# Kernel tuning notes

Hardware: AMD Instinct MI355X
Metric: run time of the kernel (lower is better)

## Reference

```python
import jax, jax.numpy as jnp
import numpy as np

NS, NC, T, NB = 32, 16, 64, 512
NSC = NS + NC


def setup_inputs() -> dict:
    key = jax.random.key(0)
    k1, k2, k3, k4, k5 = jax.random.split(key, 5)
    # SPD cost matrices so Quu is invertible (as assumed by the LQR math)
    L = jax.random.normal(k1, (NB, T, NSC, NSC), jnp.float32) * 0.1
    Q = L @ jnp.swapaxes(L, -1, -2) + jnp.eye(NSC, dtype=jnp.float32)
    p = jax.random.normal(k2, (NB, T, NSC), jnp.float32)
    x_init = jax.random.normal(k3, (NB, NS), jnp.float32)
    # stable-ish LTI dynamics
    A = 0.9 * jnp.eye(NS, dtype=jnp.float32) + 0.01 * jax.random.normal(k4, (NS, NS), jnp.float32)
    B = 0.1 * jax.random.normal(k5, (NS, NC), jnp.float32)
    dt = jnp.float32(0.1)
    return {"x_init": x_init, "Q": Q, "p": p, "A": A, "B": B, "dt": dt}


def _lqr(x_init, Q, p, A, B):
    ns, nc = A.shape[0], B.shape[1]
    nb, Th = Q.shape[0], Q.shape[1]
    dtype = Q.dtype

    # --- nominal rollout with zero control: x_{t+1} = A x_t ---
    def roll(x, _):
        return x @ A.T, x
    _, cx = jax.lax.scan(roll, x_init, None, length=Th)   # [T,B,ns] states x_0..x_{T-1}
    cu = jnp.zeros((Th, nb, nc), dtype)                    # current_u = 0
    xu = jnp.concatenate([cx, cu], -1)                     # [T,B,nsc]

    Qs = jnp.swapaxes(Q, 0, 1)                             # [T,B,nsc,nsc]
    ps = jnp.swapaxes(p, 0, 1)                             # [T,B,nsc]
    p_new = jnp.einsum('tbij,tbj->tbi', Qs, xu) + ps       # [T,B,nsc]

    F = jnp.concatenate([A, B], axis=1)                    # [ns, nsc]

    # --- backward Riccati recursion (V=v=0 at t=T-1 makes Qt=Q[T-1]) ---
    def bwd(carry, inp):
        V, v = carry                                       # [B,ns,ns], [B,ns]
        Qt_in, qt_in = inp
        Qt = Qt_in + jnp.einsum('si,bst,tj->bij', F, V, F)
        qt = qt_in + v @ F                                 # F^T v
        Qxx, Qxu = Qt[:, :ns, :ns], Qt[:, :ns, ns:]
        Qux, Quu = Qt[:, ns:, :ns], Qt[:, ns:, ns:]
        qx, qu = qt[:, :ns], qt[:, ns:]
        Quu_inv = jnp.linalg.pinv(Quu)
        Kt = -Quu_inv @ Qux                                # [B,nc,ns]
        kt = -jnp.einsum('bij,bj->bi', Quu_inv, qu)        # [B,nc]
        KtT = jnp.swapaxes(Kt, -1, -2)
        Vn = Qxx + Qxu @ Kt + KtT @ Qux + KtT @ Quu @ Kt
        vn = (qx + jnp.einsum('bij,bj->bi', Qxu, kt)
              + jnp.einsum('bij,bj->bi', KtT, qu)
              + jnp.einsum('bij,bj->bi', KtT @ Quu, kt))
        return (Vn, vn), (Kt, kt)

    V0 = jnp.zeros((nb, ns, ns), dtype)
    v0 = jnp.zeros((nb, ns), dtype)
    _, (Ks, ks) = jax.lax.scan(bwd, (V0, v0), (Qs, p_new), reverse=True)

    # --- forward rollout with feedback policy ---
    def fwd(carry, inp):
        xt, cost = carry
        Kt, kt, cxt, cut, Qt, pt = inp
        dut = jnp.einsum('bij,bj->bi', Kt, xt - cxt) + kt
        ut = dut + cut
        xut = jnp.concatenate([xt, ut], -1)
        cost = cost + 0.5 * jnp.einsum('bi,bij,bj->b', xut, Qt, xut) + (xut * pt).sum(-1)
        xn = xt @ A.T + ut @ B.T
        return (xn, cost), (xt, ut)

    (_, cost), (xs, us) = jax.lax.scan(
        fwd, (x_init, jnp.zeros(nb, dtype)), (Ks, ks, cx, cu, Qs, ps))
    x = jnp.swapaxes(xs, 0, 1)   # [B,T,ns]  (states x_0..x_{T-1}, matching x[...,:-1,:])
    u = jnp.swapaxes(us, 0, 1)   # [B,T,nc]
    return x, u, cost


def reference(x_init, Q, p, A, B, dt):
    # dt only matters for nonlinear relinearization; with constant LTI (A,B) it is unused.
    return _lqr(x_init, Q, p, A, B)
```

## Files before the change

### kernel.cpp

```cpp
#include <hip/hip_runtime.h>


#define NSd 32
#define NCd 16
#define Td 64
#define NBd 512
#define SQS 52
#define TP 40
#define FP 20

typedef __bf16 bf16x8 __attribute__((ext_vector_type(8)));
typedef __bf16 bf16x4 __attribute__((ext_vector_type(4)));
typedef float f32x4 __attribute__((ext_vector_type(4)));

#define MFMA16(a, b, c) __builtin_amdgcn_mfma_f32_16x16x32_bf16(a, b, c, 0, 0, 0)

#define XOFF ((size_t)0)
#define UOFF ((size_t)NBd * Td * NSd)
#define COFF (UOFF + (size_t)NBd * Td * NCd)

__device__ __forceinline__ float rdl(float v, int l) {
  return __uint_as_float(__builtin_amdgcn_readlane(__float_as_uint(v), l));
}

__device__ __forceinline__ void bar_lgkm() {
  asm volatile("s_waitcnt lgkmcnt(0)\n\ts_barrier" ::: "memory");
}

struct BW {
  __bf16 FTh[48][TP], FTl[48][TP];
  __bf16 WTh[48][TP], WTl[48][TP];
  __bf16 Xh[32][TP], Xl[32][TP];
  __bf16 KTh[32][TP], KTl[32][TP];
  __bf16 XTh[16][TP], XTl[16][TP];
  __bf16 S2h[48][TP], S2l[48][TP];
  float S1T[6][16][FP];
  float QdT[3][16][FP];
  float Qd1R[16][FP];
  float QuuT[16][FP];
  float qt[48];
  float vv[32];
};
struct FW {
  float K2T[2][16 * 36];
  float kv2[2][16];
  float d[32];
  float xs[32];
  float uu[16];
};
union LdsU {
  BW bw;
  FW fw;
};

#define SQSTORE(i, v)                            \
  do {                                           \
    int _r = (i) / 12, _c = (i) - _r * 12;       \
    *(float4*)&sQ[_r * SQS + _c * 4] = (v);      \
  } while (0)

__global__ __launch_bounds__(256, 2) void lqr_kernel(
    const float* __restrict__ x_init, const float* __restrict__ Qg,
    const float* __restrict__ pg, const float* __restrict__ Ag,
    const float* __restrict__ Bg, float* __restrict__ out,
    float* __restrict__ wsK, float* __restrict__ wskv) {
  const int b = blockIdx.x;
  const int tid = threadIdx.x;
  const int w = tid >> 6;
  const int lane = tid & 63;
  const int fn = lane & 15;
  const int quad = lane >> 4;
  const int k0 = quad * 8;

  __shared__ __attribute__((aligned(16))) float sQ[48 * SQS];
  __shared__ __attribute__((aligned(16))) float scx[Td][NSd];
  __shared__ __attribute__((aligned(16))) float sFf[NSd][SQS];
  __shared__ __attribute__((aligned(16))) LdsU U;
  __shared__ float scostp[1];

  for (int idx = tid; idx < 1536; idx += 256) {
    int i = idx / 48, j = idx - i * 48;
    sFf[i][j] = (j < 32) ? Ag[i * 32 + j] : Bg[i * 16 + (j - 32)];
  }
  for (int idx = tid; idx < 1536; idx += 256) {
    int a = idx >> 5, k = idx & 31;
    float f = (a < 32) ? Ag[k * 32 + a] : Bg[k * 16 + (a - 32)];
    __bf16 h = (__bf16)f;
    U.bw.FTh[a][k] = h;
    U.bw.FTl[a][k] = (__bf16)(f - (float)h);
  }
  for (int idx = tid; idx < 1536; idx += 256) {
    int r = idx >> 5, c = idx & 31;
    __bf16 z = (__bf16)0.f;
    U.bw.S2h[r][c] = z;
    U.bw.S2l[r][c] = z;
    if (r < 32) {
      U.bw.KTh[r][c] = z;
      U.bw.KTl[r][c] = z;
    }
  }
  for (int idx = tid; idx < 6 * 16 * FP; idx += 256) ((float*)U.bw.S1T)[idx] = 0.f;
  if (tid < 32) {
    scx[0][tid] = x_init[b * 32 + tid];
    U.bw.vv[tid] = 0.f;
  }
  {
    const float4* src = (const float4*)(Qg + ((size_t)b * Td + 63) * 2304);
    float4 v0 = src[tid];
    float4 v1 = src[tid + 256];
    SQSTORE(tid, v0);
    SQSTORE(tid + 256, v1);
    if (tid < 64) {
      float4 v2 = src[tid + 512];
      SQSTORE(tid + 512, v2);
    }
  }
  float ppf = 0.f;
  if (w == 3 && lane < 48) ppf = pg[((size_t)b * Td + 63) * 48 + lane];
  __syncthreads();

  if (w == 0) {
    for (int t2 = 0; t2 < Td - 1; ++t2) {
      if (lane < 32) {
        float acc = 0.f;
#pragma unroll
        for (int j = 0; j < 32; j += 4) {
          float4 a4 = *(const float4*)&sFf[lane][j];
          acc += a4.x * scx[t2][j] + a4.y * scx[t2][j + 1] +
                 a4.z * scx[t2][j + 2] + a4.w * scx[t2][j + 3];
        }
        scx[t2 + 1][lane] = acc;
      }
    }
  }
  __syncthreads();

  float cAcc = 0.f;
  float dAcc = 0.f;

  for (int t = Td - 1; t >= 0; --t) {
    float4 pf0, pf1, pf2;
    float ppfn;
    if (t > 0) {
      if (w < 3) {
        const float4* src = (const float4*)(Qg + ((size_t)b * Td + (t - 1)) * 2304);
        pf0 = src[tid];
        pf1 = src[tid + 192];
        pf2 = src[tid + 384];
      } else if (lane < 48) {
        ppfn = pg[((size_t)b * Td + t - 1) * 48 + lane];
      }
    }

    if (w < 3) {
      const int I = w;
      {
        bf16x8 aH = *(const bf16x8*)&U.bw.S2h[16 * I + fn][k0];
        bf16x8 aL = *(const bf16x8*)&U.bw.S2l[16 * I + fn][k0];
#pragma unroll
        for (int J = 0; J < 2; ++J) {
          bf16x8 bH = *(const bf16x8*)&U.bw.KTh[16 * J + fn][k0];
          bf16x8 bL = *(const bf16x8*)&U.bw.KTl[16 * J + fn][k0];
          float4 s1 = *(const float4*)&U.bw.S1T[I * 2 + J][fn][4 * quad];
          f32x4 acc = {s1.x, s1.y, s1.z, s1.w};
          acc = MFMA16(aL, bH, acc);
          acc = MFMA16(aH, bL, acc);
          acc = MFMA16(aH, bH, acc);
#pragma unroll
          for (int r = 0; r < 4; ++r) {
            float v = acc[r];
            __bf16 h = (__bf16)v;
            U.bw.WTh[16 * I + 4 * quad + r][16 * J + fn] = h;
            U.bw.WTl[16 * I + 4 * quad + r][16 * J + fn] = (__bf16)(v - (float)h);
          }
        }
      }
      bf16x8 wH = *(const bf16x8*)&U.bw.WTh[16 * I + fn][k0];
      bf16x8 wL = *(const bf16x8*)&U.bw.WTl[16 * I + fn][k0];
      if (I == 2) {
        bf16x8 bH = *(const bf16x8*)&U.bw.FTh[32 + fn][k0];
        bf16x8 bL = *(const bf16x8*)&U.bw.FTl[32 + fn][k0];
        f32x4 acc;
#pragma unroll
        for (int r = 0; r < 4; ++r)
          acc[r] = sQ[(32 + 4 * quad + r) * SQS + 32 + fn];
        acc = MFMA16(wL, bH, acc);
        acc = MFMA16(wH, bL, acc);
        acc = MFMA16(wH, bH, acc);
        float4 st = {acc[0], acc[1], acc[2], acc[3]};
        *(float4*)&U.bw.QuuT[fn][4 * quad] = st;
      } else {
        {
          bf16x8 bH = *(const bf16x8*)&U.bw.FTh[16 * I + fn][k0];
          bf16x8 bL = *(const bf16x8*)&U.bw.FTl[16 * I + fn][k0];
          f32x4 acc;
#pragma unroll
          for (int r = 0; r < 4; ++r)
            acc[r] = sQ[(16 * I + 4 * quad + r) * SQS + 16 * I + fn];
          acc = MFMA16(wL, bH, acc);
          acc = MFMA16(wH, bL, acc);
          acc = MFMA16(wH, bH, acc);
          float4 st = {acc[0], acc[1], acc[2], acc[3]};
          *(float4*)&U.bw.QdT[I * 2][fn][4 * quad] = st;
        }
        if (I == 0) {
          bf16x8 bH = *(const bf16x8*)&U.bw.FTh[16 + fn][k0];
          bf16x8 bL = *(const bf16x8*)&U.bw.FTl[16 + fn][k0];
          f32x4 acc;
#pragma unroll
          for (int r = 0; r < 4; ++r)
            acc[r] = sQ[(4 * quad + r) * SQS + 16 + fn];
          acc = MFMA16(wL, bH, acc);
          acc = MFMA16(wH, bL, acc);
          acc = MFMA16(wH, bH, acc);
          float4 st = {acc[0], acc[1], acc[2], acc[3]};
          *(float4*)&U.bw.QdT[1][fn][4 * quad] = st;
#pragma unroll
          for (int r = 0; r < 4; ++r) U.bw.Qd1R[4 * quad + r][fn] = acc[r];
        }
        {
          bf16x8 bH = *(const bf16x8*)&U.bw.FTh[32 + fn][k0];
          bf16x8 bL = *(const bf16x8*)&U.bw.FTl[32 + fn][k0];
          f32x4 acc;
#pragma unroll
          for (int r = 0; r < 4; ++r)
            acc[r] = sQ[(16 * I + 4 * quad + r) * SQS + 32 + fn];
          acc = MFMA16(wL, bH, acc);
          acc = MFMA16(wH, bL, acc);
          acc = MFMA16(wH, bH, acc);
          bf16x4 th, tl;
#pragma unroll
          for (int r = 0; r < 4; ++r) {
            float v = acc[r];
            __bf16 h = (__bf16)v;
            __bf16 l = (__bf16)(v - (float)h);
            U.bw.Xh[16 * I + 4 * quad + r][fn] = h;
            U.bw.Xl[16 * I + 4 * quad + r][fn] = l;
            th[r] = h;
            tl[r] = l;
          }
          *(bf16x4*)&U.bw.XTh[fn][16 * I + 4 * quad] = th;
          *(bf16x4*)&U.bw.XTl[fn][16 * I + 4 * quad] = tl;
        }
      }
    } else if (lane < 48) {
      float acc1 = ppf;
#pragma unroll
      for (int k = 0; k < 32; ++k) acc1 += sQ[k * SQS + lane] * scx[t][k];
      if (lane < 32) cAcc += 0.5f * scx[t][lane] * (acc1 + ppf);
      float acc = acc1;
#pragma unroll
      for (int k = 0; k < 32; ++k) acc += U.bw.vv[k] * sFf[k][lane];
      U.bw.qt[lane] = acc;
    }
    bar_lgkm();

    if (t > 0) {
      if (w < 3) {
        SQSTORE(tid, pf0);
        SQSTORE(tid + 192, pf1);
        SQSTORE(tid + 384, pf2);
      } else if (lane < 48) {
        ppf = ppfn;
      }
    }
    if (w < 3 && t > 0) {
      const int I = w;
      bf16x8 aH = *(const bf16x8*)&U.bw.FTh[16 * I + fn][k0];
      bf16x8 aL = *(const bf16x8*)&U.bw.FTl[16 * I + fn][k0];
#pragma unroll
      for (int J = 0; J < 2; ++J) {
        const float* bsrc;
        if (J == 0)
          bsrc = (quad < 2) ? &U.bw.QdT[0][fn][0] : &U.bw.Qd1R[fn][0];
        else
          bsrc = (quad < 2) ? &U.bw.QdT[1][fn][0] : &U.bw.QdT[2][fn][0];
        const int off = (quad & 1) * 8;
        float4 c0 = *(const float4*)&bsrc[off];
        float4 c1 = *(const float4*)&bsrc[off + 4];
        float bf[8] = {c0.x, c0.y, c0.z, c0.w, c1.x, c1.y, c1.z, c1.w};
        bf16x8 bH, bL;
#pragma unroll
        for (int j = 0; j < 8; ++j) {
          __bf16 h = (__bf16)bf[j];
          bH[j] = h;
          bL[j] = (__bf16)(bf[j] - (float)h);
        }
        f32x4 acc = {0.f, 0.f, 0.f, 0.f};
        acc = MFMA16(aL, bH, acc);
        acc = MFMA16(aH, bL, acc);
        acc = MFMA16(aH, bH, acc);
        float4 st = {acc[0], acc[1], acc[2], acc[3]};
        *(float4*)&U.bw.S1T[I * 2 + J][fn][4 * quad] = st;
      }
      {
        bf16x8 bH = *(const bf16x8*)&U.bw.XTh[fn][k0];
        bf16x8 bL = *(const bf16x8*)&U.bw.XTl[fn][k0];
        f32x4 acc = {0.f, 0.f, 0.f, 0.f};
        acc = MFMA16(aL, bH, acc);
        acc = MFMA16(aH, bL, acc);
        acc = MFMA16(aH, bH, acc);
#pragma unroll
        for (int r = 0; r < 4; ++r) {
          float v = acc[r];
          __bf16 h = (__bf16)v;
          U.bw.S2h[16 * I + 4 * quad + r][fn] = h;
          U.bw.S2l[16 * I + 4 * quad + r][fn] = (__bf16)(v - (float)h);
        }
      }
    }
    if (w == 3) {
      float rhs[16];
      if (lane < 32) {
        bf16x8 xh0 = *(const bf16x8*)&U.bw.Xh[lane][0];
        bf16x8 xh1 = *(const bf16x8*)&U.bw.Xh[lane][8];
        bf16x8 xl0 = *(const bf16x8*)&U.bw.Xl[lane][0];
        bf16x8 xl1 = *(const bf16x8*)&U.bw.Xl[lane][8];
#pragma unroll
        for (int i = 0; i < 8; ++i) {
          rhs[i] = (float)xh0[i] + (float)xl0[i];
          rhs[8 + i] = (float)xh1[i] + (float)xl1[i];
        }
      } else {
#pragma unroll
        for (int i = 0; i < 16; ++i) rhs[i] = U.bw.qt[32 + i];
      }
      float quu[16];
      *(float4*)&quu[0] = *(const float4*)&U.bw.QuuT[fn][0];
      *(float4*)&quu[4] = *(const float4*)&U.bw.QuuT[fn][4];
      *(float4*)&quu[8] = *(const float4*)&U.bw.QuuT[fn][8];
      *(float4*)&quu[12] = *(const float4*)&U.bw.QuuT[fn][12];
      float inv[16];
#pragma unroll
      for (int r = 0; r < 15; ++r) {
        inv[r] = __builtin_amdgcn_rcpf(rdl(quu[r], r));
#pragma unroll
        for (int i = r + 1; i < 16; ++i) {
          float m = rdl(quu[i], r) * inv[r];
          rhs[i] -= m * rhs[r];
          quu[i] -= m * quu[r];
        }
      }
      inv[15] = __builtin_amdgcn_rcpf(rdl(quu[15], 15));
      float xx[16];
#pragma unroll
      for (int r = 15; r >= 0; --r) {
        float s = rhs[r];
#pragma unroll
        for (int c = r + 1; c < 16; ++c) s -= rdl(quu[r], c) * xx[c];
        xx[r] = s * inv[r];
      }
      if (lane < 32) {
        bf16x8 h0, l0, h1, l1;
#pragma unroll
        for (int u = 0; u < 8; ++u) {
          float kv = -xx[u];
          __bf16 hh = (__bf16)kv;
          h0[u] = hh;
          l0[u] = (__bf16)(kv - (float)hh);
          float kv2 = -xx[8 + u];
          __bf16 hh2 = (__bf16)kv2;
          h1[u] = hh2;
          l1[u] = (__bf16)(kv2 - (float)hh2);
        }
        *(bf16x8*)&U.bw.KTh[lane][0] = h0;
        *(bf16x8*)&U.bw.KTh[lane][8] = h1;
        *(bf16x8*)&U.bw.KTl[lane][0] = l0;
        *(bf16x8*)&U.bw.KTl[lane][8] = l1;
        float4* dst = (float4*)(wsK + (((size_t)b * Td + t) * 32 + lane) * 16);
        float4 v0 = {-xx[0], -xx[1], -xx[2], -xx[3]};
        float4 v1 = {-xx[4], -xx[5], -xx[6], -xx[7]};
        float4 v2 = {-xx[8], -xx[9], -xx[10], -xx[11]};
        float4 v3 = {-xx[12], -xx[13], -xx[14], -xx[15]};
        dst[0] = v0; dst[1] = v1; dst[2] = v2; dst[3] = v3;
      } else if (lane == 32) {
        float4* dst = (float4*)(wskv + ((size_t)b * Td + t) * 16);
        float4 v0 = {-xx[0], -xx[1], -xx[2], -xx[3]};
        float4 v1 = {-xx[4], -xx[5], -xx[6], -xx[7]};
        float4 v2 = {-xx[8], -xx[9], -xx[10], -xx[11]};
        float4 v3 = {-xx[12], -xx[13], -xx[14], -xx[15]};
        dst[0] = v0; dst[1] = v1; dst[2] = v2; dst[3] = v3;
        float s = 0.f;
#pragma unroll
        for (int i = 0; i < 16; ++i) s += U.bw.qt[32 + i] * xx[i];
        dAcc -= 0.5f * s;
      }
      {
        float acc = 0.f;
        bf16x8 xh0, xh1, xl0, xl1;
        if (lane < 32) {
          xh0 = *(const bf16x8*)&U.bw.Xh[lane][0];
          xh1 = *(const bf16x8*)&U.bw.Xh[lane][8];
          xl0 = *(const bf16x8*)&U.bw.Xl[lane][0];
          xl1 = *(const bf16x8*)&U.bw.Xl[lane][8];
          acc = U.bw.qt[lane];
        }
#pragma unroll
        for (int u = 0; u < 8; ++u) {
          float kt0 = -rdl(xx[u], 32);
          float kt1 = -rdl(xx[8 + u], 32);
          if (lane < 32) {
            acc += ((float)xh0[u] + (float)xl0[u]) * kt0;
            acc += ((float)xh1[u] + (float)xl1[u]) * kt1;
          }
        }
        if (lane < 32) U.bw.vv[lane] = acc;
      }
    }
    bar_lgkm();
  }

  if (w == 3) {
    float rv = (lane < 32) ? cAcc : (lane == 32 ? dAcc : 0.f);
    rv += __shfl_down(rv, 32);
    rv += __shfl_down(rv, 16);
    rv += __shfl_down(rv, 8);
    rv += __shfl_down(rv, 4);
    rv += __shfl_down(rv, 2);
    rv += __shfl_down(rv, 1);
    if (lane == 0) scostp[0] = rv;
  }
  __syncthreads();

  if (w == 0) {
    {
      const float4* src = (const float4*)(wsK + ((size_t)b * Td) * 512);
      float4 ka = src[lane * 2], kb = src[lane * 2 + 1];
      int jj = lane >> 1, ib = (lane & 1) * 8;
      float* kt2 = U.fw.K2T[0];
      kt2[(ib + 0) * 36 + jj] = ka.x; kt2[(ib + 1) * 36 + jj] = ka.y;
      kt2[(ib + 2) * 36 + jj] = ka.z; kt2[(ib + 3) * 36 + jj] = ka.w;
      kt2[(ib + 4) * 36 + jj] = kb.x; kt2[(ib + 5) * 36 + jj] = kb.y;
      kt2[(ib + 6) * 36 + jj] = kb.z; kt2[(ib + 7) * 36 + jj] = kb.w;
      if (lane < 16) U.fw.kv2[0][lane] = wskv[(size_t)b * Td * 16 + lane];
    }
    float xr = (lane < 32) ? scx[0][lane] : 0.f;
    for (int t = 0; t < Td; ++t) {
      const int cur = t & 1, nxt = cur ^ 1;
      float4 pa, pb;
      float pk;
      if (t < Td - 1) {
        const float4* src = (const float4*)(wsK + ((size_t)b * Td + t + 1) * 512);
        pa = src[lane * 2];
        pb = src[lane * 2 + 1];
        if (lane < 16) pk = wskv[((size_t)b * Td + t + 1) * 16 + lane];
      }
      if (lane < 32) {
        U.fw.d[lane] = xr - scx[t][lane];
        U.fw.xs[lane] = xr;
        out[XOFF + ((size_t)b * Td + t) * 32 + lane] = xr;
      }
      if (lane < 16) {
        float uv = U.fw.kv2[cur][lane];
        const float* kr = &U.fw.K2T[cur][lane * 36];
#pragma unroll
        for (int j4 = 0; j4 < 8; ++j4) {
          float4 kk = *(const float4*)&kr[j4 * 4];
          float4 dd = *(const float4*)&U.fw.d[j4 * 4];
          uv += kk.x * dd.x + kk.y * dd.y + kk.z * dd.z + kk.w * dd.w;
        }
        U.fw.uu[lane] = uv;
        out[UOFF + ((size_t)b * Td + t) * 16 + lane] = uv;
      }
      if (lane < 32) {
        float acc = 0.f;
#pragma unroll
        for (int j4 = 0; j4 < 8; ++j4) {
          float4 ff = *(const float4*)&sFf[lane][j4 * 4];
          float4 xv = *(const float4*)&U.fw.xs[j4 * 4];
          acc += ff.x * xv.x + ff.y * xv.y + ff.z * xv.z + ff.w * xv.w;
        }
#pragma unroll
        for (int j4 = 0; j4 < 4; ++j4) {
          float4 ff = *(const float4*)&sFf[lane][32 + j4 * 4];
          float4 uv = *(const float4*)&U.fw.uu[j4 * 4];
          acc += ff.x * uv.x + ff.y * uv.y + ff.z * uv.z + ff.w * uv.w;
        }
        xr = acc;
      }
      if (t < Td - 1) {
        int jj = lane >> 1, ib = (lane & 1) * 8;
        float* kt2 = U.fw.K2T[nxt];
        kt2[(ib + 0) * 36 + jj] = pa.x; kt2[(ib + 1) * 36 + jj] = pa.y;
        kt2[(ib + 2) * 36 + jj] = pa.z; kt2[(ib + 3) * 36 + jj] = pa.w;
        kt2[(ib + 4) * 36 + jj] = pb.x; kt2[(ib + 5) * 36 + jj] = pb.y;
        kt2[(ib + 6) * 36 + jj] = pb.z; kt2[(ib + 7) * 36 + jj] = pb.w;
        if (lane < 16) U.fw.kv2[nxt][lane] = pk;
      }
    }
    if (lane == 0) out[COFF + b] = scostp[0];
  }
}

extern "C" void kernel_launch(void* const* d_in, const int* in_sizes, int n_in,
                              void* d_out, int out_size, void* d_ws, size_t ws_size,
                              hipStream_t stream) {
  const float* x_init = (const float*)d_in[0];
  const float* Qg = (const float*)d_in[1];
  const float* pg = (const float*)d_in[2];
  const float* Ag = (const float*)d_in[3];
  const float* Bg = (const float*)d_in[4];
  float* out = (float*)d_out;
  float* wsK = (float*)d_ws;
  float* wskv = wsK + (size_t)NBd * Td * NSd * NCd;
  lqr_kernel<<<NBd, 256, 0, stream>>>(x_init, Qg, pg, Ag, Bg, out, wsK, wskv);
}
```

Before: 620.8 us.

## Rotate wave roles per block and hoist loop-invariant MFMA operands into registers

Wave roles are rotated by a block-dependent shift so the serial solver wave lands on different SIMDs across co-resident blocks. Loop-invariant bf16 F^T fragments, F columns, and the carried S1/S2 fragments are kept in registers instead of being reloaded from LDS each step. The solver wave also gets raised priority, the q-vector is read once into registers, and the sQ access is vectorized. The v update is rewritten algebraically from Qxu*k to a dot of the solve result with qu. This adds register pressure, and the v-update algebra depends on what xx holds for lanes below 32.

```diff
diff --git a/kernel.cpp b/kernel.cpp
--- a/kernel.cpp
+++ b/kernel.cpp
@@ -71,6 +71,8 @@
   const int fn = lane & 15;
   const int quad = lane >> 4;
   const int k0 = quad * 8;
+  const int shift = (b ^ (b >> 8)) & 3;
+  const int rw = (w + shift) & 3;
 
   __shared__ __attribute__((aligned(16))) float sQ[48 * SQS];
   __shared__ __attribute__((aligned(16))) float scx[Td][NSd];
@@ -116,10 +118,10 @@
     }
   }
   float ppf = 0.f;
-  if (w == 3 && lane < 48) ppf = pg[((size_t)b * Td + 63) * 48 + lane];
+  if (rw == 3 && lane < 48) ppf = pg[((size_t)b * Td + 63) * 48 + lane];
   __syncthreads();
 
-  if (w == 0) {
+  if (rw == 0) {
     for (int t2 = 0; t2 < Td - 1; ++t2) {
       if (lane < 32) {
         float acc = 0.f;
@@ -135,6 +137,23 @@
   }
   __syncthreads();
 
+  const int I3 = (rw < 3) ? rw : 0;
+  bf16x8 hFTdH = *(const bf16x8*)&U.bw.FTh[16 * I3 + fn][k0];
+  bf16x8 hFTdL = *(const bf16x8*)&U.bw.FTl[16 * I3 + fn][k0];
+  bf16x8 hFT1H = *(const bf16x8*)&U.bw.FTh[16 + fn][k0];
+  bf16x8 hFT1L = *(const bf16x8*)&U.bw.FTl[16 + fn][k0];
+  bf16x8 hFT2H = *(const bf16x8*)&U.bw.FTh[32 + fn][k0];
+  bf16x8 hFT2L = *(const bf16x8*)&U.bw.FTl[32 + fn][k0];
+  bf16x8 hS2H = *(const bf16x8*)&U.bw.S2h[16 * I3 + fn][k0];
+  bf16x8 hS2L = *(const bf16x8*)&U.bw.S2l[16 * I3 + fn][k0];
+  float4 hS1a = *(const float4*)&U.bw.S1T[I3 * 2 + 0][fn][4 * quad];
+  float4 hS1b = *(const float4*)&U.bw.S1T[I3 * 2 + 1][fn][4 * quad];
+  float fcol[32];
+  if (rw == 3 && lane < 48) {
+#pragma unroll
+    for (int k = 0; k < 32; ++k) fcol[k] = sFf[k][lane];
+  }
+
   float cAcc = 0.f;
   float dAcc = 0.f;
 
@@ -142,30 +161,29 @@
     float4 pf0, pf1, pf2;
     float ppfn;
     if (t > 0) {
-      if (w < 3) {
+      if (rw < 3) {
+        const int ptid = rw * 64 + lane;
         const float4* src = (const float4*)(Qg + ((size_t)b * Td + (t - 1)) * 2304);
-        pf0 = src[tid];
-        pf1 = src[tid + 192];
-        pf2 = src[tid + 384];
+        pf0 = src[ptid];
+        pf1 = src[ptid + 192];
+        pf2 = src[ptid + 384];
       } else if (lane < 48) {
         ppfn = pg[((size_t)b * Td + t - 1) * 48 + lane];
       }
     }
 
-    if (w < 3) {
-      const int I = w;
+    if (rw < 3) {
+      const int I = rw;
       {
-        bf16x8 aH = *(const bf16x8*)&U.bw.S2h[16 * I + fn][k0];
-        bf16x8 aL = *(const bf16x8*)&U.bw.S2l[16 * I + fn][k0];
 #pragma unroll
         for (int J = 0; J < 2; ++J) {
           bf16x8 bH = *(const bf16x8*)&U.bw.KTh[16 * J + fn][k0];
           bf16x8 bL = *(const bf16x8*)&U.bw.KTl[16 * J + fn][k0];
-          float4 s1 = *(const float4*)&U.bw.S1T[I * 2 + J][fn][4 * quad];
+          float4 s1 = (J == 0) ? hS1a : hS1b;
           f32x4 acc = {s1.x, s1.y, s1.z, s1.w};
-          acc = MFMA16(aL, bH, acc);
-          acc = MFMA16(aH, bL, acc);
-          acc = MFMA16(aH, bH, acc);
+          acc = MFMA16(hS2L, bH, acc);
+          acc = MFMA16(hS2H, bL, acc);
+          acc = MFMA16(hS2H, bH, acc);
 #pragma unroll
           for (int r = 0; r < 4; ++r) {
             float v = acc[r];
@@ -178,56 +196,50 @@
       bf16x8 wH = *(const bf16x8*)&U.bw.WTh[16 * I + fn][k0];
       bf16x8 wL = *(const bf16x8*)&U.bw.WTl[16 * I + fn][k0];
       if (I == 2) {
-        bf16x8 bH = *(const bf16x8*)&U.bw.FTh[32 + fn][k0];
-        bf16x8 bL = *(const bf16x8*)&U.bw.FTl[32 + fn][k0];
         f32x4 acc;
 #pragma unroll
         for (int r = 0; r < 4; ++r)
           acc[r] = sQ[(32 + 4 * quad + r) * SQS + 32 + fn];
-        acc = MFMA16(wL, bH, acc);
-        acc = MFMA16(wH, bL, acc);
-        acc = MFMA16(wH, bH, acc);
+        acc = MFMA16(wL, hFT2H, acc);
+        acc = MFMA16(wH, hFT2L, acc);
+        acc = MFMA16(wH, hFT2H, acc);
         float4 st = {acc[0], acc[1], acc[2], acc[3]};
         *(float4*)&U.bw.QuuT[fn][4 * quad] = st;
       } else {
         {
-          bf16x8 bH = *(const bf16x8*)&U.bw.FTh[16 * I + fn][k0];
-          bf16x8 bL = *(const bf16x8*)&U.bw.FTl[16 * I + fn][k0];
+          bf16x8 dH = (I == 0) ? hFTdH : hFT1H;
+          bf16x8 dL = (I == 0) ? hFTdL : hFT1L;
           f32x4 acc;
 #pragma unroll
           for (int r = 0; r < 4; ++r)
             acc[r] = sQ[(16 * I + 4 * quad + r) * SQS + 16 * I + fn];
-          acc = MFMA16(wL, bH, acc);
-          acc = MFMA16(wH, bL, acc);
-          acc = MFMA16(wH, bH, acc);
+          acc = MFMA16(wL, dH, acc);
+          acc = MFMA16(wH, dL, acc);
+          acc = MFMA16(wH, dH, acc);
           float4 st = {acc[0], acc[1], acc[2], acc[3]};
           *(float4*)&U.bw.QdT[I * 2][fn][4 * quad] = st;
         }
         if (I == 0) {
-          bf16x8 bH = *(const bf16x8*)&U.bw.FTh[16 + fn][k0];
-          bf16x8 bL = *(const bf16x8*)&U.bw.FTl[16 + fn][k0];
           f32x4 acc;
 #pragma unroll
           for (int r = 0; r < 4; ++r)
             acc[r] = sQ[(4 * quad + r) * SQS + 16 + fn];
-          acc = MFMA16(wL, bH, acc);
-          acc = MFMA16(wH, bL, acc);
-          acc = MFMA16(wH, bH, acc);
+          acc = MFMA16(wL, hFT1H, acc);
+          acc = MFMA16(wH, hFT1L, acc);
+          acc = MFMA16(wH, hFT1H, acc);
           float4 st = {acc[0], acc[1], acc[2], acc[3]};
           *(float4*)&U.bw.QdT[1][fn][4 * quad] = st;
 #pragma unroll
           for (int r = 0; r < 4; ++r) U.bw.Qd1R[4 * quad + r][fn] = acc[r];
         }
         {
-          bf16x8 bH = *(const bf16x8*)&U.bw.FTh[32 + fn][k0];
-          bf16x8 bL = *(const bf16x8*)&U.bw.FTl[32 + fn][k0];
           f32x4 acc;
 #pragma unroll
           for (int r = 0; r < 4; ++r)
             acc[r] = sQ[(16 * I + 4 * quad + r) * SQS + 32 + fn];
-          acc = MFMA16(wL, bH, acc);
-          acc = MFMA16(wH, bL, acc);
-          acc = MFMA16(wH, bH, acc);
+          acc = MFMA16(wL, hFT2H, acc);
+          acc = MFMA16(wH, hFT2L, acc);
+          acc = MFMA16(wH, hFT2H, acc);
           bf16x4 th, tl;
 #pragma unroll
           for (int r = 0; r < 4; ++r) {
@@ -246,28 +258,31 @@
     } else if (lane < 48) {
       float acc1 = ppf;
 #pragma unroll
-      for (int k = 0; k < 32; ++k) acc1 += sQ[k * SQS + lane] * scx[t][k];
+      for (int j = 0; j < 8; ++j) {
+        float4 q4 = *(const float4*)&sQ[lane * SQS + j * 4];
+        acc1 += q4.x * scx[t][j * 4] + q4.y * scx[t][j * 4 + 1] +
+                q4.z * scx[t][j * 4 + 2] + q4.w * scx[t][j * 4 + 3];
+      }
       if (lane < 32) cAcc += 0.5f * scx[t][lane] * (acc1 + ppf);
       float acc = acc1;
 #pragma unroll
-      for (int k = 0; k < 32; ++k) acc += U.bw.vv[k] * sFf[k][lane];
+      for (int k = 0; k < 32; ++k) acc += U.bw.vv[k] * fcol[k];
       U.bw.qt[lane] = acc;
     }
     bar_lgkm();
 
     if (t > 0) {
-      if (w < 3) {
-        SQSTORE(tid, pf0);
-        SQSTORE(tid + 192, pf1);
-        SQSTORE(tid + 384, pf2);
+      if (rw < 3) {
+        const int ptid = rw * 64 + lane;
+        SQSTORE(ptid, pf0);
+        SQSTORE(ptid + 192, pf1);
+        SQSTORE(ptid + 384, pf2);
       } else if (lane < 48) {
         ppf = ppfn;
       }
     }
-    if (w < 3 && t > 0) {
-      const int I = w;
-      bf16x8 aH = *(const bf16x8*)&U.bw.FTh[16 * I + fn][k0];
-      bf16x8 aL = *(const bf16x8*)&U.bw.FTl[16 * I + fn][k0];
+    if (rw < 3 && t > 0) {
+      const int I = rw;
 #pragma unroll
       for (int J = 0; J < 2; ++J) {
         const float* bsrc;
@@ -287,9 +302,9 @@
           bL[j] = (__bf16)(bf[j] - (float)h);
         }
         f32x4 acc = {0.f, 0.f, 0.f, 0.f};
-        acc = MFMA16(aL, bH, acc);
-        acc = MFMA16(aH, bL, acc);
-        acc = MFMA16(aH, bH, acc);
+        acc = MFMA16(hFTdL, bH, acc);
+        acc = MFMA16(hFTdH, bL, acc);
+        acc = MFMA16(hFTdH, bH, acc);
         float4 st = {acc[0], acc[1], acc[2], acc[3]};
         *(float4*)&U.bw.S1T[I * 2 + J][fn][4 * quad] = st;
       }
@@ -297,9 +312,9 @@
         bf16x8 bH = *(const bf16x8*)&U.bw.XTh[fn][k0];
         bf16x8 bL = *(const bf16x8*)&U.bw.XTl[fn][k0];
         f32x4 acc = {0.f, 0.f, 0.f, 0.f};
-        acc = MFMA16(aL, bH, acc);
-        acc = MFMA16(aH, bL, acc);
-        acc = MFMA16(aH, bH, acc);
+        acc = MFMA16(hFTdL, bH, acc);
+        acc = MFMA16(hFTdH, bL, acc);
+        acc = MFMA16(hFTdH, bH, acc);
 #pragma unroll
         for (int r = 0; r < 4; ++r) {
           float v = acc[r];
@@ -308,8 +323,18 @@
           U.bw.S2l[16 * I + 4 * quad + r][fn] = (__bf16)(v - (float)h);
         }
       }
-    }
-    if (w == 3) {
+      hS2H = *(const bf16x8*)&U.bw.S2h[16 * I + fn][k0];
+      hS2L = *(const bf16x8*)&U.bw.S2l[16 * I + fn][k0];
+      hS1a = *(const float4*)&U.bw.S1T[I * 2 + 0][fn][4 * quad];
+      hS1b = *(const float4*)&U.bw.S1T[I * 2 + 1][fn][4 * quad];
+    }
+    if (rw == 3) {
+      __builtin_amdgcn_s_setprio(1);
+      float quv[16];
+      *(float4*)&quv[0] = *(const float4*)&U.bw.qt[32];
+      *(float4*)&quv[4] = *(const float4*)&U.bw.qt[36];
+      *(float4*)&quv[8] = *(const float4*)&U.bw.qt[40];
+      *(float4*)&quv[12] = *(const float4*)&U.bw.qt[44];
       float rhs[16];
       if (lane < 32) {
         bf16x8 xh0 = *(const bf16x8*)&U.bw.Xh[lane][0];
@@ -323,7 +348,7 @@
         }
       } else {
 #pragma unroll
-        for (int i = 0; i < 16; ++i) rhs[i] = U.bw.qt[32 + i];
+        for (int i = 0; i < 16; ++i) rhs[i] = quv[i];
       }
       float quu[16];
       *(float4*)&quu[0] = *(const float4*)&U.bw.QuuT[fn][0];
@@ -382,35 +407,21 @@
         dst[0] = v0; dst[1] = v1; dst[2] = v2; dst[3] = v3;
         float s = 0.f;
 #pragma unroll
-        for (int i = 0; i < 16; ++i) s += U.bw.qt[32 + i] * xx[i];
+        for (int i = 0; i < 16; ++i) s += quv[i] * xx[i];
         dAcc -= 0.5f * s;
       }
-      {
-        float acc = 0.f;
-        bf16x8 xh0, xh1, xl0, xl1;
-        if (lane < 32) {
-          xh0 = *(const bf16x8*)&U.bw.Xh[lane][0];
-          xh1 = *(const bf16x8*)&U.bw.Xh[lane][8];
-          xl0 = *(const bf16x8*)&U.bw.Xl[lane][0];
-          xl1 = *(const bf16x8*)&U.bw.Xl[lane][8];
-          acc = U.bw.qt[lane];
-        }
-#pragma unroll
-        for (int u = 0; u < 8; ++u) {
-          float kt0 = -rdl(xx[u], 32);
-          float kt1 = -rdl(xx[8 + u], 32);
-          if (lane < 32) {
-            acc += ((float)xh0[u] + (float)xl0[u]) * kt0;
-            acc += ((float)xh1[u] + (float)xl1[u]) * kt1;
-          }
-        }
-        if (lane < 32) U.bw.vv[lane] = acc;
-      }
+      if (lane < 32) {
+        float acc = U.bw.qt[lane];
+#pragma unroll
+        for (int i = 0; i < 16; ++i) acc -= xx[i] * quv[i];
+        U.bw.vv[lane] = acc;
+      }
+      __builtin_amdgcn_s_setprio(0);
     }
     bar_lgkm();
   }
 
-  if (w == 3) {
+  if (rw == 3) {
     float rv = (lane < 32) ? cAcc : (lane == 32 ? dAcc : 0.f);
     rv += __shfl_down(rv, 32);
     rv += __shfl_down(rv, 16);
@@ -422,7 +433,7 @@
   }
   __syncthreads();
 
-  if (w == 0) {
+  if (rw == 0) {
     {
       const float4* src = (const float4*)(wsK + ((size_t)b * Td) * 512);
       float4 ka = src[lane * 2], kb = src[lane * 2 + 1];
```

New measurement: 630.8 us. Within noise of the previous version (+1.6%).
